# Kernel tuning notes

Measured on AMD Instinct MI355X. Metric: run time of the kernel, lower is better.

The kernel has to match this reference:

```python
import jax, jax.numpy as jnp
import numpy as np

B, T, F, D, NCLS = 32, 1024, 128, 64, 11
EPS = 1e-3  # keras BatchNormalization default epsilon


def sinusoidal_pe(t, f, dtype=jnp.float32):
    pos = jnp.arange(t, dtype=jnp.float32)[:, None]                      # [T,1]
    div = jnp.exp(-jnp.log(10000.0) * jnp.arange(0, f, 2, dtype=jnp.float32) / f)
    ang = pos * div                                                      # [T,F/2]
    pe = jnp.zeros((t, f), dtype=jnp.float32)
    pe = pe.at[:, 0::2].set(jnp.sin(ang)).at[:, 1::2].set(jnp.cos(ang))
    return pe.astype(dtype)


def setup_inputs() -> dict:
    key = jax.random.key(0)
    ks = jax.random.split(key, 18)
    s = 0.05
    return {
        "x": jax.random.normal(ks[0], (B, T, F), jnp.float32),
        "wq": jax.random.normal(ks[1], (F, D), jnp.float32) * s,
        "wk": jax.random.normal(ks[2], (F, D), jnp.float32) * s,
        "wv": jax.random.normal(ks[3], (F, D), jnp.float32) * s,
        "bn_a_gamma": jax.random.uniform(ks[4], (D,), jnp.float32, 0.5, 1.5),
        "bn_a_beta": jax.random.normal(ks[5], (D,), jnp.float32) * s,
        "bn_a_mean": jax.random.normal(ks[6], (D,), jnp.float32) * s,
        "bn_a_var": jax.random.uniform(ks[7], (D,), jnp.float32, 0.5, 1.5),
        "w0": jax.random.normal(ks[8], (D, 64), jnp.float32) * s,
        "b0": jax.random.normal(ks[9], (64,), jnp.float32) * s,
        "w1": jax.random.normal(ks[10], (F, 64), jnp.float32) * s,
        "b1": jax.random.normal(ks[11], (64,), jnp.float32) * s,
        "bn1_gamma": jax.random.uniform(ks[12], (128,), jnp.float32, 0.5, 1.5),
        "bn1_beta": jax.random.normal(ks[13], (128,), jnp.float32) * s,
        "bn1_mean": jax.random.normal(ks[14], (128,), jnp.float32) * s,
        "bn1_var": jax.random.uniform(ks[15], (128,), jnp.float32, 0.5, 1.5),
        "wd": jax.random.normal(ks[16], (128, NCLS), jnp.float32) * s,
        "bd": jax.random.normal(ks[17], (NCLS,), jnp.float32) * s,
    }


def _bn(h, gamma, beta, mean, var):
    # inference-mode batch norm over last axis
    return (h - mean) * (gamma * jax.lax.rsqrt(var + EPS)) + beta


def reference(x, wq, wk, wv, bn_a_gamma, bn_a_beta, bn_a_mean, bn_a_var,
              w0, b0, w1, b1, bn1_gamma, bn1_beta, bn1_mean, bn1_var, wd, bd):
    # AttentionLayer: positional encoding + single-head scaled dot-product attention
    xp = x + sinusoidal_pe(x.shape[1], x.shape[2], x.dtype)              # [B,T,F]
    q = jnp.einsum("btf,fd->btd", xp, wq)
    k = jnp.einsum("btf,fd->btd", xp, wk)
    v = jnp.einsum("btf,fd->btd", xp, wv)
    scores = jnp.einsum("bqd,bkd->bqk", q, k) / jnp.sqrt(jnp.float32(D))  # [B,T,T]
    attn = jax.nn.softmax(scores, axis=-1)
    x1 = jnp.einsum("bqk,bkd->bqd", attn, v)                             # [B,T,D]
    x1 = _bn(x1, bn_a_gamma, bn_a_beta, bn_a_mean, bn_a_var)
    # per-timestep heads (vectorized over T)
    out1 = jax.nn.relu(jnp.einsum("btd,de->bte", x1, w0) + b0)           # [B,T,64]
    out2 = jax.nn.relu(jnp.einsum("btf,fe->bte", x, w1) + b1)            # [B,T,64]
    h = jnp.concatenate([out1, out2], axis=-1)                           # [B,T,128]
    h = _bn(h, bn1_gamma, bn1_beta, bn1_mean, bn1_var)
    # dropout is identity in inference mode
    logits = jnp.einsum("bte,ec->btc", h, wd) + bd                       # [B,T,11]
    return jax.nn.softmax(logits, axis=-1)
```

## Files before the change

kernel.cpp:

```cpp
#include <hip/hip_runtime.h>
#include <math.h>

#define BB 32
#define TT 1024
#define FF 128
#define DD 64
#define NCLS 11
constexpr float kEps = 1e-3f;
constexpr int M = BB * TT;

typedef __attribute__((ext_vector_type(8))) short short8v;
typedef __attribute__((ext_vector_type(4))) short short4v;
typedef __attribute__((ext_vector_type(4))) float float4v;

__device__ __forceinline__ short f2bf(float f) {
  union { float f; unsigned u; } v; v.f = f;
  return (short)((v.u + 0x7FFFu + ((v.u >> 16) & 1u)) >> 16);
}
__device__ __forceinline__ float bf2f(short s) {
  union { unsigned u; float f; } v; v.u = ((unsigned)(unsigned short)s) << 16;
  return v.f;
}

__global__ __launch_bounds__(256) void prep_kernel(
    const float* __restrict__ wq, const float* __restrict__ wk,
    const float* __restrict__ wv, const float* __restrict__ w1,
    const float* __restrict__ w0, const float* __restrict__ b0,
    const float* __restrict__ bn_a_gamma, const float* __restrict__ bn_a_beta,
    const float* __restrict__ bn_a_mean, const float* __restrict__ bn_a_var,
    const float* __restrict__ bn1_gamma, const float* __restrict__ bn1_beta,
    const float* __restrict__ bn1_mean, const float* __restrict__ bn1_var,
    const float* __restrict__ wd, const float* __restrict__ bd,
    short* __restrict__ wT4,
    short* __restrict__ w0pT, float* __restrict__ b0p,
    short* __restrict__ wdpT, float* __restrict__ bdp,
    float* __restrict__ peq, float* __restrict__ pek, float* __restrict__ pev) {
  const int t = threadIdx.x;
  const int blk = blockIdx.x;

  if (blk >= 5) {
    __shared__ float peL[16][128];
    const int p = blk - 5;
    const int y = p >> 6;
    const int t0 = (p & 63) * 16;
#pragma unroll
    for (int i = 0; i < 8; ++i) {
      const int idx = t + i * 256;
      const int tr = idx >> 7, f = idx & 127;
      const float div = expf(-logf(10000.0f) * (float)(f & ~1) / (float)FF);
      const float ang = (float)(t0 + tr) * div;
      peL[tr][f] = (f & 1) ? cosf(ang) : sinf(ang);
    }
    __syncthreads();
    const float* w = (y == 0) ? wq : (y == 1) ? wk : wv;
    float* dst = (y == 0) ? peq : (y == 1) ? pek : pev;
    const int tr = t >> 4, dq = t & 15;
    float4 acc = {0.f, 0.f, 0.f, 0.f};
    for (int f = 0; f < FF; ++f) {
      const float pv = peL[tr][f];
      const float4 w4 = *(const float4*)&w[f * 64 + dq * 4];
      acc.x += pv * w4.x; acc.y += pv * w4.y;
      acc.z += pv * w4.z; acc.w += pv * w4.w;
    }
    *(float4*)&dst[(t0 + tr) * 64 + dq * 4] = acc;
    return;
  }
  if (blk > 0) {
    const int y = blk - 1;
    const float* w = (y == 0) ? wq : (y == 1) ? wk : (y == 2) ? wv : w1;
    short* dst = wT4 + y * 8192;
#pragma unroll
    for (int i = 0; i < 4; ++i) {
      const int idx = t + i * 256;
      const int n = idx >> 4, c = idx & 15;
      short8v s8;
#pragma unroll
      for (int j = 0; j < 8; ++j) s8[j] = f2bf(w[(c * 8 + j) * 64 + n]);
      *(short8v*)&dst[n * 128 + ((c ^ (n & 7)) << 3)] = s8;
    }
    return;
  }
  __shared__ float cA[64], cAo[64], c1s[64], c1o[64], c2s[64], c2o[64];
  if (t < 64) {
    const float sA = bn_a_gamma[t] * rsqrtf(bn_a_var[t] + kEps);
    cA[t] = sA; cAo[t] = bn_a_beta[t] - bn_a_mean[t] * sA;
    const float s1 = bn1_gamma[t] * rsqrtf(bn1_var[t] + kEps);
    c1s[t] = s1; c1o[t] = bn1_beta[t] - bn1_mean[t] * s1;
    const float s2 = bn1_gamma[t + 64] * rsqrtf(bn1_var[t + 64] + kEps);
    c2s[t] = s2; c2o[t] = bn1_beta[t + 64] - bn1_mean[t + 64] * s2;
  }
  __syncthreads();
  for (int i = t; i < 4096; i += 256) {
    const int e = i >> 6, k = i & 63;
    w0pT[i] = f2bf(cA[k] * w0[k * 64 + e]);
  }
  if (t < 64) {
    float s = b0[t];
    for (int k = 0; k < 64; ++k) s += cAo[k] * w0[k * 64 + t];
    b0p[t] = s;
  }
  for (int i = t; i < 2048; i += 256) {
    const int c = i >> 7, e = i & 127;
    float v = 0.f;
    if (c < NCLS) v = wd[e * NCLS + c] * (e < 64 ? c1s[e] : c2s[e - 64]);
    wdpT[i] = f2bf(v);
  }
  if (t < 16) {
    float s = 0.f;
    if (t < NCLS) {
      s = bd[t];
      for (int e = 0; e < 64; ++e) s += c1o[e] * wd[e * NCLS + t];
      for (int e = 0; e < 64; ++e) s += c2o[e] * wd[(64 + e) * NCLS + t];
    }
    bdp[t] = s;
  }
}

__global__ __launch_bounds__(256) void proj_kernel(
    const float* __restrict__ x, const short* __restrict__ wT4,
    const float* __restrict__ peq, const float* __restrict__ pek,
    const float* __restrict__ pev, const float* __restrict__ b1,
    short* __restrict__ qo, short* __restrict__ ko,
    short* __restrict__ vt, short* __restrict__ o2) {
  __shared__ __align__(16) short xs[128 * 128];
  __shared__ __align__(16) short wsh[64 * 128];
  const int tid = threadIdx.x;
  const int lane = tid & 63;
  const int wv4 = tid >> 6;
  const int l15 = lane & 15;
  const int lg = lane >> 4;
  const int r0 = blockIdx.x * 128;
  const int y = blockIdx.y;

#pragma unroll
  for (int i = 0; i < 8; ++i) {
    int id = tid + i * 256;
    int row = id >> 4, chunk = id & 15;
    const float* xp = &x[((size_t)(r0 + row)) * FF + chunk * 8];
    const float4 a = *(const float4*)xp;
    const float4 b = *(const float4*)(xp + 4);
    short8v s8;
    s8[0] = f2bf(a.x); s8[1] = f2bf(a.y); s8[2] = f2bf(a.z); s8[3] = f2bf(a.w);
    s8[4] = f2bf(b.x); s8[5] = f2bf(b.y); s8[6] = f2bf(b.z); s8[7] = f2bf(b.w);
    *(short8v*)&xs[row * 128 + ((chunk ^ (row & 7)) << 3)] = s8;
  }
#pragma unroll
  for (int i = 0; i < 4; ++i) {
    const int idx = tid + i * 256;
    *(int4*)&wsh[idx * 8] = *(const int4*)&wT4[y * 8192 + idx * 8];
  }
  __syncthreads();

  float4v acc[2][4];
#pragma unroll
  for (int rt = 0; rt < 2; ++rt)
#pragma unroll
    for (int dt = 0; dt < 4; ++dt) acc[rt][dt] = (float4v)0.0f;

  const bool natural = (y == 2);
#pragma unroll
  for (int kt = 0; kt < 4; ++kt) {
    const int chunk = kt * 4 + lg;
    short8v xa[2], wa[4];
#pragma unroll
    for (int rt = 0; rt < 2; ++rt) {
      const int row = wv4 * 32 + rt * 16 + l15;
      xa[rt] = *(const short8v*)&xs[row * 128 + ((chunk ^ (row & 7)) << 3)];
    }
#pragma unroll
    for (int dt = 0; dt < 4; ++dt) {
      const int n = dt * 16 + l15;
      wa[dt] = *(const short8v*)&wsh[n * 128 + ((chunk ^ (n & 7)) << 3)];
    }
#pragma unroll
    for (int rt = 0; rt < 2; ++rt)
#pragma unroll
      for (int dt = 0; dt < 4; ++dt)
        acc[rt][dt] = natural
            ? __builtin_amdgcn_mfma_f32_16x16x32_bf16(xa[rt], wa[dt], acc[rt][dt], 0, 0, 0)
            : __builtin_amdgcn_mfma_f32_16x16x32_bf16(wa[dt], xa[rt], acc[rt][dt], 0, 0, 0);
  }

  if (natural) {
    const int bq = r0 >> 10;
    const int tb = (r0 & 1023) + wv4 * 32;
#pragma unroll
    for (int rt = 0; rt < 2; ++rt) {
#pragma unroll
      for (int dt = 0; dt < 4; ++dt) {
        const int d = dt * 16 + l15;
        const int t0 = tb + rt * 16 + lg * 4;
        short4v s;
#pragma unroll
        for (int r = 0; r < 4; ++r)
          s[r] = f2bf(acc[rt][dt][r] + pev[(t0 + r) * 64 + d]);
        *(short4v*)&vt[((size_t)(bq * DD + d)) * TT + t0] = s;
      }
    }
  } else {
    short* dst = (y == 0) ? qo : (y == 1) ? ko : o2;
    const float* petab = (y == 0) ? peq : pek;
#pragma unroll
    for (int rt = 0; rt < 2; ++rt) {
      const int row = r0 + wv4 * 32 + rt * 16 + l15;
      const int tr = row & 1023;
#pragma unroll
      for (int dt = 0; dt < 4; ++dt) {
        const int d0 = dt * 16 + lg * 4;
        float v0 = acc[rt][dt][0], v1 = acc[rt][dt][1];
        float v2 = acc[rt][dt][2], v3 = acc[rt][dt][3];
        if (y == 3) {
          const float4 bv = *(const float4*)&b1[d0];
          v0 = fmaxf(v0 + bv.x, 0.f); v1 = fmaxf(v1 + bv.y, 0.f);
          v2 = fmaxf(v2 + bv.z, 0.f); v3 = fmaxf(v3 + bv.w, 0.f);
        } else {
          const float4 pv = *(const float4*)&petab[tr * 64 + d0];
          v0 += pv.x; v1 += pv.y; v2 += pv.z; v3 += pv.w;
        }
        short4v s;
        s[0] = f2bf(v0); s[1] = f2bf(v1); s[2] = f2bf(v2); s[3] = f2bf(v3);
        *(short4v*)&dst[(size_t)row * DD + d0] = s;
      }
    }
  }
}

__global__ __launch_bounds__(256) void attn_head_kernel(
    const short* __restrict__ qg, const short* __restrict__ kg,
    const short* __restrict__ vtg, const short* __restrict__ o2m,
    const short* __restrict__ w0pT, const float* __restrict__ b0p,
    const short* __restrict__ wdpT, const float* __restrict__ bdp,
    float* __restrict__ out) {
  __shared__ __align__(16) short Ks[2][64 * 64];
  __shared__ __align__(16) short Vs[2][64 * 64];
  __shared__ __align__(16) short Ps[4 * 16 * 64];
  const int tid = threadIdx.x;
  const int lane = tid & 63;
  const int wv = tid >> 6;
  const int b = blockIdx.y;
  const int qx = blockIdx.x;
  const int l15 = lane & 15;
  const int lg = lane >> 4;
  const int qbase = qx * 64 + wv * 16;

  const int srow0 = tid >> 3, sc8 = (tid & 7) * 8;
  const int ssw = sc8 ^ ((srow0 & 7) << 3);
  const int srow1 = (tid + 256) >> 3;
  const int ssw1 = sc8 ^ ((srow1 & 7) << 3);

  short8v qf[2];
#pragma unroll
  for (int dt = 0; dt < 2; ++dt) {
    const size_t off = ((size_t)(b * TT + qbase + l15)) * DD + dt * 32 + lg * 8;
    qf[dt] = *(const short8v*)&qg[off];
  }
  float4v oacc[4];
#pragma unroll
  for (int dt = 0; dt < 4; ++dt) oacc[dt] = (float4v)0.0f;
  float lacc[4] = {0.f, 0.f, 0.f, 0.f};

  {
    const int4 k0 = *(const int4*)&kg[((size_t)(b * TT + srow0)) * DD + sc8];
    const int4 v0 = *(const int4*)&vtg[((size_t)(b * DD + srow0)) * TT + sc8];
    const int4 k1 = *(const int4*)&kg[((size_t)(b * TT + srow1)) * DD + sc8];
    const int4 v1 = *(const int4*)&vtg[((size_t)(b * DD + srow1)) * TT + sc8];
    *(int4*)&Ks[0][srow0 * 64 + ssw] = k0;
    *(int4*)&Vs[0][srow0 * 64 + ssw] = v0;
    *(int4*)&Ks[0][srow1 * 64 + ssw1] = k1;
    *(int4*)&Vs[0][srow1 * 64 + ssw1] = v1;
  }
  __syncthreads();

  const int pbase = wv * 1024;
  for (int kt = 0; kt < 16; ++kt) {
    const int cur = kt & 1;

    int4 nk0, nv0, nk1, nv1;
    if (kt < 15) {
      const int nt = (kt + 1) * 64;
      nk0 = *(const int4*)&kg[((size_t)(b * TT + nt + srow0)) * DD + sc8];
      nv0 = *(const int4*)&vtg[((size_t)(b * DD + srow0)) * TT + nt + sc8];
      nk1 = *(const int4*)&kg[((size_t)(b * TT + nt + srow1)) * DD + sc8];
      nv1 = *(const int4*)&vtg[((size_t)(b * DD + srow1)) * TT + nt + sc8];
    }

    short8v kf[8];
#pragma unroll
    for (int jt = 0; jt < 4; ++jt) {
      const int j = jt * 16 + l15;
#pragma unroll
      for (int dt = 0; dt < 2; ++dt) {
        const int d0 = dt * 32 + lg * 8;
        kf[jt * 2 + dt] = *(const short8v*)&Ks[cur][j * 64 + (d0 ^ ((j & 7) << 3))];
      }
    }
    float4v s[4];
#pragma unroll
    for (int jt = 0; jt < 4; ++jt) {
      s[jt] = (float4v)0.0f;
      s[jt] = __builtin_amdgcn_mfma_f32_16x16x32_bf16(qf[0], kf[jt * 2 + 0], s[jt], 0, 0, 0);
      s[jt] = __builtin_amdgcn_mfma_f32_16x16x32_bf16(qf[1], kf[jt * 2 + 1], s[jt], 0, 0, 0);
    }

#pragma unroll
    for (int jt = 0; jt < 4; ++jt) {
      const int j = jt * 16 + l15;
#pragma unroll
      for (int r = 0; r < 4; ++r) {
        const float pv = __expf(s[jt][r] * 0.125f);
        lacc[r] += pv;
        const int i = lg * 4 + r;
        Ps[pbase + i * 64 + (j ^ ((i & 7) << 3))] = f2bf(pv);
      }
    }

    short8v pf[2];
#pragma unroll
    for (int jc = 0; jc < 2; ++jc) {
      const int j0 = jc * 32 + lg * 8;
      pf[jc] = *(const short8v*)&Ps[pbase + l15 * 64 + (j0 ^ ((l15 & 7) << 3))];
    }
    short8v vf[8];
#pragma unroll
    for (int dt = 0; dt < 4; ++dt) {
      const int d = dt * 16 + l15;
#pragma unroll
      for (int jc = 0; jc < 2; ++jc) {
        const int j0 = jc * 32 + lg * 8;
        vf[dt * 2 + jc] = *(const short8v*)&Vs[cur][d * 64 + (j0 ^ ((d & 7) << 3))];
      }
    }
#pragma unroll
    for (int dt = 0; dt < 4; ++dt) {
      oacc[dt] = __builtin_amdgcn_mfma_f32_16x16x32_bf16(pf[0], vf[dt * 2 + 0], oacc[dt], 0, 0, 0);
      oacc[dt] = __builtin_amdgcn_mfma_f32_16x16x32_bf16(pf[1], vf[dt * 2 + 1], oacc[dt], 0, 0, 0);
    }

    if (kt < 15) {
      *(int4*)&Ks[cur ^ 1][srow0 * 64 + ssw] = nk0;
      *(int4*)&Vs[cur ^ 1][srow0 * 64 + ssw] = nv0;
      *(int4*)&Ks[cur ^ 1][srow1 * 64 + ssw1] = nk1;
      *(int4*)&Vs[cur ^ 1][srow1 * 64 + ssw1] = nv1;
      __syncthreads();
    }
  }

#pragma unroll
  for (int off = 1; off < 16; off <<= 1) {
#pragma unroll
    for (int r = 0; r < 4; ++r) lacc[r] += __shfl_xor(lacc[r], off);
  }

  short* hs = &Ps[pbase];

#pragma unroll
  for (int r = 0; r < 4; ++r) {
    const int m = lg * 4 + r;
#pragma unroll
    for (int dt = 0; dt < 4; ++dt) {
      const int chunk = (dt * 2 + (l15 >> 3)) ^ (m & 7);
      hs[m * 64 + chunk * 8 + (l15 & 7)] = f2bf(oacc[dt][r]);
    }
  }

  short8v af[2];
#pragma unroll
  for (int dt = 0; dt < 2; ++dt) {
    const int chunk = (dt * 4 + lg) ^ (l15 & 7);
    af[dt] = *(const short8v*)&hs[l15 * 64 + chunk * 8];
  }

  float4v acc1[4];
#pragma unroll
  for (int et = 0; et < 4; ++et) acc1[et] = (float4v)0.0f;
#pragma unroll
  for (int et = 0; et < 4; ++et)
#pragma unroll
    for (int dt = 0; dt < 2; ++dt) {
      const short8v wb = *(const short8v*)&w0pT[(et * 16 + l15) * 64 + dt * 32 + lg * 8];
      acc1[et] = __builtin_amdgcn_mfma_f32_16x16x32_bf16(af[dt], wb, acc1[et], 0, 0, 0);
    }

  float b0v[4];
#pragma unroll
  for (int et = 0; et < 4; ++et) b0v[et] = b0p[et * 16 + l15];

#pragma unroll
  for (int r = 0; r < 4; ++r) {
    const float invm = 1.0f / lacc[r];
    const int m = lg * 4 + r;
#pragma unroll
    for (int et = 0; et < 4; ++et) {
      const float v = fmaxf(acc1[et][r] * invm + b0v[et], 0.f);
      const int chunk = (et * 2 + (l15 >> 3)) ^ (m & 7);
      hs[m * 64 + chunk * 8 + (l15 & 7)] = f2bf(v);
    }
  }

  float4v accL = (float4v)0.0f;
#pragma unroll
  for (int dt = 0; dt < 2; ++dt) {
    const int chunk = (dt * 4 + lg) ^ (l15 & 7);
    const short8v ha = *(const short8v*)&hs[l15 * 64 + chunk * 8];
    const short8v wb = *(const short8v*)&wdpT[l15 * 128 + dt * 32 + lg * 8];
    accL = __builtin_amdgcn_mfma_f32_16x16x32_bf16(ha, wb, accL, 0, 0, 0);
  }
  const size_t o2row = ((size_t)b * TT + qbase + l15) * DD;
#pragma unroll
  for (int dt = 0; dt < 2; ++dt) {
    const short8v ha = *(const short8v*)&o2m[o2row + dt * 32 + lg * 8];
    const short8v wb = *(const short8v*)&wdpT[l15 * 128 + 64 + dt * 32 + lg * 8];
    accL = __builtin_amdgcn_mfma_f32_16x16x32_bf16(ha, wb, accL, 0, 0, 0);
  }

  const float bdv = bdp[l15];
#pragma unroll
  for (int r = 0; r < 4; ++r) {
    const float lv = (l15 < NCLS) ? (accL[r] + bdv) : -1e30f;
    float mx = lv;
#pragma unroll
    for (int off = 1; off < 16; off <<= 1) mx = fmaxf(mx, __shfl_xor(mx, off));
    const float ex = (l15 < NCLS) ? __expf(lv - mx) : 0.f;
    float sm = ex;
#pragma unroll
    for (int off = 1; off < 16; off <<= 1) sm += __shfl_xor(sm, off);
    if (l15 < NCLS)
      out[((size_t)b * TT + qbase + lg * 4 + r) * NCLS + l15] = ex / sm;
  }
}

extern "C" void kernel_launch(void* const* d_in, const int* in_sizes, int n_in,
                              void* d_out, int out_size, void* d_ws, size_t ws_size,
                              hipStream_t stream) {
  (void)in_sizes; (void)n_in; (void)out_size; (void)ws_size;
  const float* x  = (const float*)d_in[0];
  const float* wq = (const float*)d_in[1];
  const float* wk = (const float*)d_in[2];
  const float* wv = (const float*)d_in[3];
  const float* bn_a_gamma = (const float*)d_in[4];
  const float* bn_a_beta  = (const float*)d_in[5];
  const float* bn_a_mean  = (const float*)d_in[6];
  const float* bn_a_var   = (const float*)d_in[7];
  const float* w0 = (const float*)d_in[8];
  const float* b0 = (const float*)d_in[9];
  const float* w1 = (const float*)d_in[10];
  const float* b1 = (const float*)d_in[11];
  const float* bn1_gamma = (const float*)d_in[12];
  const float* bn1_beta  = (const float*)d_in[13];
  const float* bn1_mean  = (const float*)d_in[14];
  const float* bn1_var   = (const float*)d_in[15];
  const float* wd = (const float*)d_in[16];
  const float* bd = (const float*)d_in[17];
  float* out = (float*)d_out;

  char* cur = (char*)d_ws;
  short* q  = (short*)cur; cur += (size_t)M * DD * 2;
  short* k  = (short*)cur; cur += (size_t)M * DD * 2;
  short* vt = (short*)cur; cur += (size_t)M * DD * 2;
  short* o2 = (short*)cur; cur += (size_t)M * DD * 2;
  short* wT4  = (short*)cur; cur += 4 * 8192 * 2;
  short* w0pT = (short*)cur; cur += 4096 * 2;
  short* wdpT = (short*)cur; cur += 2048 * 2;
  float* b0p  = (float*)cur; cur += 64 * 4;
  float* bdp  = (float*)cur; cur += 16 * 4;
  float* peq  = (float*)cur; cur += (size_t)TT * DD * 4;
  float* pek  = (float*)cur; cur += (size_t)TT * DD * 4;
  float* pev  = (float*)cur; cur += (size_t)TT * DD * 4;

  prep_kernel<<<dim3(197), dim3(256), 0, stream>>>(
      wq, wk, wv, w1, w0, b0, bn_a_gamma, bn_a_beta, bn_a_mean, bn_a_var,
      bn1_gamma, bn1_beta, bn1_mean, bn1_var, wd, bd,
      wT4, w0pT, b0p, wdpT, bdp, peq, pek, pev);
  proj_kernel<<<dim3(M / 128, 4), dim3(256), 0, stream>>>(
      x, wT4, peq, pek, pev, b1, q, k, vt, o2);
  attn_head_kernel<<<dim3(TT / 64, BB), dim3(256), 0, stream>>>(
      q, k, vt, o2, w0pT, b0p, wdpT, bdp, out);
}
```

Measured before the change: 56.41 us.

## Split attention key range across two wave groups per block with LDS merge

The attention kernel now runs 512 threads per block as two groups of four waves, each processing half of the key tiles for the same 64 queries. The partial output accumulators and row sums are merged through LDS before one group runs the head MLP and softmax. Block indices are also remapped so that consecutive blocks interleave batches. The intent is to shorten the serial key loop per block and raise the number of waves in flight. The cost is extra LDS traffic, an added barrier, and half of the waves sitting idle during the epilogue.

```diff
diff --git a/kernel.cpp b/kernel.cpp
--- a/kernel.cpp
+++ b/kernel.cpp
@@ -225,33 +225,38 @@
   }
 }
 
-__global__ __launch_bounds__(256) void attn_head_kernel(
+__global__ __launch_bounds__(512, 4) void attn_head_kernel(
     const short* __restrict__ qg, const short* __restrict__ kg,
     const short* __restrict__ vtg, const short* __restrict__ o2m,
     const short* __restrict__ w0pT, const float* __restrict__ b0p,
     const short* __restrict__ wdpT, const float* __restrict__ bdp,
     float* __restrict__ out) {
-  __shared__ __align__(16) short Ks[2][64 * 64];
-  __shared__ __align__(16) short Vs[2][64 * 64];
-  __shared__ __align__(16) short Ps[4 * 16 * 64];
+  __shared__ __align__(16) short Ks[2][2][4096];
+  __shared__ __align__(16) short Vs[2][2][4096];
+  __shared__ __align__(16) short Ps[8 * 1024];
   const int tid = threadIdx.x;
   const int lane = tid & 63;
-  const int wv = tid >> 6;
-  const int b = blockIdx.y;
-  const int qx = blockIdx.x;
+  const int wid = tid >> 6;
+  const int grp = wid >> 2;
+  const int wv = wid & 3;
+  const int id = blockIdx.x;
+  const int bb = (id & 7) + ((id >> 7) << 3);
+  const int qx = (id >> 3) & 15;
   const int l15 = lane & 15;
   const int lg = lane >> 4;
   const int qbase = qx * 64 + wv * 16;
-
-  const int srow0 = tid >> 3, sc8 = (tid & 7) * 8;
+  const int kt0 = grp * 8;
+
+  const int stid = tid & 255;
+  const int srow0 = stid >> 3, sc8 = (stid & 7) * 8;
   const int ssw = sc8 ^ ((srow0 & 7) << 3);
-  const int srow1 = (tid + 256) >> 3;
+  const int srow1 = srow0 + 32;
   const int ssw1 = sc8 ^ ((srow1 & 7) << 3);
 
   short8v qf[2];
 #pragma unroll
   for (int dt = 0; dt < 2; ++dt) {
-    const size_t off = ((size_t)(b * TT + qbase + l15)) * DD + dt * 32 + lg * 8;
+    const size_t off = ((size_t)(bb * TT + qbase + l15)) * DD + dt * 32 + lg * 8;
     qf[dt] = *(const short8v*)&qg[off];
   }
   float4v oacc[4];
@@ -260,28 +265,29 @@
   float lacc[4] = {0.f, 0.f, 0.f, 0.f};
 
   {
-    const int4 k0 = *(const int4*)&kg[((size_t)(b * TT + srow0)) * DD + sc8];
-    const int4 v0 = *(const int4*)&vtg[((size_t)(b * DD + srow0)) * TT + sc8];
-    const int4 k1 = *(const int4*)&kg[((size_t)(b * TT + srow1)) * DD + sc8];
-    const int4 v1 = *(const int4*)&vtg[((size_t)(b * DD + srow1)) * TT + sc8];
-    *(int4*)&Ks[0][srow0 * 64 + ssw] = k0;
-    *(int4*)&Vs[0][srow0 * 64 + ssw] = v0;
-    *(int4*)&Ks[0][srow1 * 64 + ssw1] = k1;
-    *(int4*)&Vs[0][srow1 * 64 + ssw1] = v1;
+    const int nt = kt0 * 64;
+    const int4 k0 = *(const int4*)&kg[((size_t)(bb * TT + nt + srow0)) * DD + sc8];
+    const int4 v0 = *(const int4*)&vtg[((size_t)(bb * DD + srow0)) * TT + nt + sc8];
+    const int4 k1 = *(const int4*)&kg[((size_t)(bb * TT + nt + srow1)) * DD + sc8];
+    const int4 v1 = *(const int4*)&vtg[((size_t)(bb * DD + srow1)) * TT + nt + sc8];
+    *(int4*)&Ks[grp][0][srow0 * 64 + ssw] = k0;
+    *(int4*)&Vs[grp][0][srow0 * 64 + ssw] = v0;
+    *(int4*)&Ks[grp][0][srow1 * 64 + ssw1] = k1;
+    *(int4*)&Vs[grp][0][srow1 * 64 + ssw1] = v1;
   }
   __syncthreads();
 
-  const int pbase = wv * 1024;
-  for (int kt = 0; kt < 16; ++kt) {
-    const int cur = kt & 1;
+  const int pbase = wid * 1024;
+  for (int i = 0; i < 8; ++i) {
+    const int cur = i & 1;
 
     int4 nk0, nv0, nk1, nv1;
-    if (kt < 15) {
-      const int nt = (kt + 1) * 64;
-      nk0 = *(const int4*)&kg[((size_t)(b * TT + nt + srow0)) * DD + sc8];
-      nv0 = *(const int4*)&vtg[((size_t)(b * DD + srow0)) * TT + nt + sc8];
-      nk1 = *(const int4*)&kg[((size_t)(b * TT + nt + srow1)) * DD + sc8];
-      nv1 = *(const int4*)&vtg[((size_t)(b * DD + srow1)) * TT + nt + sc8];
+    if (i < 7) {
+      const int nt = (kt0 + i + 1) * 64;
+      nk0 = *(const int4*)&kg[((size_t)(bb * TT + nt + srow0)) * DD + sc8];
+      nv0 = *(const int4*)&vtg[((size_t)(bb * DD + srow0)) * TT + nt + sc8];
+      nk1 = *(const int4*)&kg[((size_t)(bb * TT + nt + srow1)) * DD + sc8];
+      nv1 = *(const int4*)&vtg[((size_t)(bb * DD + srow1)) * TT + nt + sc8];
     }
 
     short8v kf[8];
@@ -291,7 +297,7 @@
 #pragma unroll
       for (int dt = 0; dt < 2; ++dt) {
         const int d0 = dt * 32 + lg * 8;
-        kf[jt * 2 + dt] = *(const short8v*)&Ks[cur][j * 64 + (d0 ^ ((j & 7) << 3))];
+        kf[jt * 2 + dt] = *(const short8v*)&Ks[grp][cur][j * 64 + (d0 ^ ((j & 7) << 3))];
       }
     }
     float4v s[4];
@@ -309,8 +315,8 @@
       for (int r = 0; r < 4; ++r) {
         const float pv = __expf(s[jt][r] * 0.125f);
         lacc[r] += pv;
-        const int i = lg * 4 + r;
-        Ps[pbase + i * 64 + (j ^ ((i & 7) << 3))] = f2bf(pv);
+        const int i2 = lg * 4 + r;
+        Ps[pbase + i2 * 64 + (j ^ ((i2 & 7) << 3))] = f2bf(pv);
       }
     }
 
@@ -327,7 +333,7 @@
 #pragma unroll
       for (int jc = 0; jc < 2; ++jc) {
         const int j0 = jc * 32 + lg * 8;
-        vf[dt * 2 + jc] = *(const short8v*)&Vs[cur][d * 64 + (j0 ^ ((d & 7) << 3))];
+        vf[dt * 2 + jc] = *(const short8v*)&Vs[grp][cur][d * 64 + (j0 ^ ((d & 7) << 3))];
       }
     }
 #pragma unroll
@@ -336,11 +342,11 @@
       oacc[dt] = __builtin_amdgcn_mfma_f32_16x16x32_bf16(pf[1], vf[dt * 2 + 1], oacc[dt], 0, 0, 0);
     }
 
-    if (kt < 15) {
-      *(int4*)&Ks[cur ^ 1][srow0 * 64 + ssw] = nk0;
-      *(int4*)&Vs[cur ^ 1][srow0 * 64 + ssw] = nv0;
-      *(int4*)&Ks[cur ^ 1][srow1 * 64 + ssw1] = nk1;
-      *(int4*)&Vs[cur ^ 1][srow1 * 64 + ssw1] = nv1;
+    if (i < 7) {
+      *(int4*)&Ks[grp][cur ^ 1][srow0 * 64 + ssw] = nk0;
+      *(int4*)&Vs[grp][cur ^ 1][srow0 * 64 + ssw] = nv0;
+      *(int4*)&Ks[grp][cur ^ 1][srow1 * 64 + ssw1] = nk1;
+      *(int4*)&Vs[grp][cur ^ 1][srow1 * 64 + ssw1] = nv1;
       __syncthreads();
     }
   }
@@ -351,81 +357,106 @@
     for (int r = 0; r < 4; ++r) lacc[r] += __shfl_xor(lacc[r], off);
   }
 
-  short* hs = &Ps[pbase];
-
-#pragma unroll
-  for (int r = 0; r < 4; ++r) {
-    const int m = lg * 4 + r;
-#pragma unroll
-    for (int dt = 0; dt < 4; ++dt) {
-      const int chunk = (dt * 2 + (l15 >> 3)) ^ (m & 7);
-      hs[m * 64 + chunk * 8 + (l15 & 7)] = f2bf(oacc[dt][r]);
-    }
-  }
-
-  short8v af[2];
-#pragma unroll
-  for (int dt = 0; dt < 2; ++dt) {
-    const int chunk = (dt * 4 + lg) ^ (l15 & 7);
-    af[dt] = *(const short8v*)&hs[l15 * 64 + chunk * 8];
-  }
-
-  float4v acc1[4];
-#pragma unroll
-  for (int et = 0; et < 4; ++et) acc1[et] = (float4v)0.0f;
-#pragma unroll
-  for (int et = 0; et < 4; ++et)
+  __syncthreads();
+  float* cb = (float*)&Ks[0][0][0];
+  float* lcb = cb + 4096;
+  if (grp == 1) {
+#pragma unroll
+    for (int r = 0; r < 4; ++r) {
+      const int m = lg * 4 + r;
+#pragma unroll
+      for (int dt = 0; dt < 4; ++dt)
+        cb[wv * 1024 + m * 64 + dt * 16 + l15] = oacc[dt][r];
+      lcb[wv * 16 + m] = lacc[r];
+    }
+  }
+  __syncthreads();
+  if (grp == 0) {
+#pragma unroll
+    for (int r = 0; r < 4; ++r) {
+      const int m = lg * 4 + r;
+#pragma unroll
+      for (int dt = 0; dt < 4; ++dt)
+        oacc[dt][r] += cb[wv * 1024 + m * 64 + dt * 16 + l15];
+      lacc[r] += lcb[wv * 16 + m];
+    }
+
+    short* hs = &Ps[pbase];
+
+#pragma unroll
+    for (int r = 0; r < 4; ++r) {
+      const int m = lg * 4 + r;
+#pragma unroll
+      for (int dt = 0; dt < 4; ++dt) {
+        const int chunk = (dt * 2 + (l15 >> 3)) ^ (m & 7);
+        hs[m * 64 + chunk * 8 + (l15 & 7)] = f2bf(oacc[dt][r]);
+      }
+    }
+
+    short8v af[2];
 #pragma unroll
     for (int dt = 0; dt < 2; ++dt) {
-      const short8v wb = *(const short8v*)&w0pT[(et * 16 + l15) * 64 + dt * 32 + lg * 8];
-      acc1[et] = __builtin_amdgcn_mfma_f32_16x16x32_bf16(af[dt], wb, acc1[et], 0, 0, 0);
-    }
-
-  float b0v[4];
-#pragma unroll
-  for (int et = 0; et < 4; ++et) b0v[et] = b0p[et * 16 + l15];
-
-#pragma unroll
-  for (int r = 0; r < 4; ++r) {
-    const float invm = 1.0f / lacc[r];
-    const int m = lg * 4 + r;
-#pragma unroll
-    for (int et = 0; et < 4; ++et) {
-      const float v = fmaxf(acc1[et][r] * invm + b0v[et], 0.f);
-      const int chunk = (et * 2 + (l15 >> 3)) ^ (m & 7);
-      hs[m * 64 + chunk * 8 + (l15 & 7)] = f2bf(v);
-    }
-  }
-
-  float4v accL = (float4v)0.0f;
-#pragma unroll
-  for (int dt = 0; dt < 2; ++dt) {
-    const int chunk = (dt * 4 + lg) ^ (l15 & 7);
-    const short8v ha = *(const short8v*)&hs[l15 * 64 + chunk * 8];
-    const short8v wb = *(const short8v*)&wdpT[l15 * 128 + dt * 32 + lg * 8];
-    accL = __builtin_amdgcn_mfma_f32_16x16x32_bf16(ha, wb, accL, 0, 0, 0);
-  }
-  const size_t o2row = ((size_t)b * TT + qbase + l15) * DD;
-#pragma unroll
-  for (int dt = 0; dt < 2; ++dt) {
-    const short8v ha = *(const short8v*)&o2m[o2row + dt * 32 + lg * 8];
-    const short8v wb = *(const short8v*)&wdpT[l15 * 128 + 64 + dt * 32 + lg * 8];
-    accL = __builtin_amdgcn_mfma_f32_16x16x32_bf16(ha, wb, accL, 0, 0, 0);
-  }
-
-  const float bdv = bdp[l15];
-#pragma unroll
-  for (int r = 0; r < 4; ++r) {
-    const float lv = (l15 < NCLS) ? (accL[r] + bdv) : -1e30f;
-    float mx = lv;
-#pragma unroll
-    for (int off = 1; off < 16; off <<= 1) mx = fmaxf(mx, __shfl_xor(mx, off));
-    const float ex = (l15 < NCLS) ? __expf(lv - mx) : 0.f;
-    float sm = ex;
-#pragma unroll
-    for (int off = 1; off < 16; off <<= 1) sm += __shfl_xor(sm, off);
-    if (l15 < NCLS)
-      out[((size_t)b * TT + qbase + lg * 4 + r) * NCLS + l15] = ex / sm;
+      const int chunk = (dt * 4 + lg) ^ (l15 & 7);
+      af[dt] = *(const short8v*)&hs[l15 * 64 + chunk * 8];
+    }
+
+    float4v acc1[4];
+#pragma unroll
+    for (int et = 0; et < 4; ++et) acc1[et] = (float4v)0.0f;
+#pragma unroll
+    for (int et = 0; et < 4; ++et)
+#pragma unroll
+      for (int dt = 0; dt < 2; ++dt) {
+        const short8v wb = *(const short8v*)&w0pT[(et * 16 + l15) * 64 + dt * 32 + lg * 8];
+        acc1[et] = __builtin_amdgcn_mfma_f32_16x16x32_bf16(af[dt], wb, acc1[et], 0, 0, 0);
+      }
+
+    float b0v[4];
+#pragma unroll
+    for (int et = 0; et < 4; ++et) b0v[et] = b0p[et * 16 + l15];
+
+#pragma unroll
+    for (int r = 0; r < 4; ++r) {
+      const float invm = 1.0f / lacc[r];
+      const int m = lg * 4 + r;
+#pragma unroll
+      for (int et = 0; et < 4; ++et) {
+        const float v = fmaxf(acc1[et][r] * invm + b0v[et], 0.f);
+        const int chunk = (et * 2 + (l15 >> 3)) ^ (m & 7);
+        hs[m * 64 + chunk * 8 + (l15 & 7)] = f2bf(v);
+      }
+    }
+
+    float4v accL = (float4v)0.0f;
+#pragma unroll
+    for (int dt = 0; dt < 2; ++dt) {
+      const int chunk = (dt * 4 + lg) ^ (l15 & 7);
+      const short8v ha = *(const short8v*)&hs[l15 * 64 + chunk * 8];
+      const short8v wb = *(const short8v*)&wdpT[l15 * 128 + dt * 32 + lg * 8];
+      accL = __builtin_amdgcn_mfma_f32_16x16x32_bf16(ha, wb, accL, 0, 0, 0);
+    }
+    const size_t o2row = ((size_t)bb * TT + qbase + l15) * DD;
+#pragma unroll
+    for (int dt = 0; dt < 2; ++dt) {
+      const short8v ha = *(const short8v*)&o2m[o2row + dt * 32 + lg * 8];
+      const short8v wb = *(const short8v*)&wdpT[l15 * 128 + 64 + dt * 32 + lg * 8];
+      accL = __builtin_amdgcn_mfma_f32_16x16x32_bf16(ha, wb, accL, 0, 0, 0);
+    }
+
+    const float bdv = bdp[l15];
+#pragma unroll
+    for (int r = 0; r < 4; ++r) {
+      const float lv = (l15 < NCLS) ? (accL[r] + bdv) : -1e30f;
+      float mx = lv;
+#pragma unroll
+      for (int off = 1; off < 16; off <<= 1) mx = fmaxf(mx, __shfl_xor(mx, off));
+      const float ex = (l15 < NCLS) ? __expf(lv - mx) : 0.f;
+      float sm = ex;
+#pragma unroll
+      for (int off = 1; off < 16; off <<= 1) sm += __shfl_xor(sm, off);
+      if (l15 < NCLS)
+        out[((size_t)bb * TT + qbase + lg * 4 + r) * NCLS + l15] = ex / sm;
+    }
   }
 }
 
@@ -473,6 +504,6 @@
       wT4, w0pT, b0p, wdpT, bdp, peq, pek, pev);
   proj_kernel<<<dim3(M / 128, 4), dim3(256), 0, stream>>>(
       x, wT4, peq, pek, pev, b1, q, k, vt, o2);
-  attn_head_kernel<<<dim3(TT / 64, BB), dim3(256), 0, stream>>>(
+  attn_head_kernel<<<dim3(512), dim3(512), 0, stream>>>(
       q, k, vt, o2, w0pT, b0p, wdpT, bdp, out);
 }
```

Measured after the change: 52.59 us. 6.8% less time.
